# Optimization experiments

Hardware: AMD Instinct MI355X
Metric: run time of the kernel (lower is better)

## Reference

```python
import jax, jax.numpy as jnp
import numpy as np

DT = 0.05          # LiquidTimeBlock dt
EPS_TAU = 1e-6     # eps added to tau
EPS_CONV = 1e-3    # ContinuousRecurrentCore epsilon
MAX_T = 50         # max_sim_time
N_LAYERS = 4


def stable_sigmoid(v):
    # Sigmoid(x) == 0.5 * (tanh(x/2) + 1)
    return 0.5 * (jnp.tanh(v * 0.5) + 1.0)


def setup_inputs() -> dict:
    key = jax.random.key(0)
    B, S, H = 8, 1024, 1024
    ks = jax.random.split(key, 7)
    bnd = 1.0 / np.sqrt(H)      # nn.Linear default init bound, fan_in=H
    bnd2 = 1.0 / np.sqrt(2 * H)  # fan_in=2H for tau_gate
    x = jax.random.normal(ks[0], (B, S, H), jnp.float32)
    w_state = jax.random.uniform(ks[1], (N_LAYERS, H, H), jnp.float32, -bnd, bnd)
    b_state = jax.random.uniform(ks[2], (N_LAYERS, H), jnp.float32, -bnd, bnd)
    w_input = jax.random.uniform(ks[3], (N_LAYERS, H, H), jnp.float32, -bnd, bnd)
    b_input = jax.random.uniform(ks[4], (N_LAYERS, H), jnp.float32, -bnd, bnd)
    w_tau = jax.random.uniform(ks[5], (N_LAYERS, H, 2 * H), jnp.float32, -bnd2, bnd2)
    b_tau = jax.random.uniform(ks[6], (N_LAYERS, H), jnp.float32, -bnd2, bnd2)
    return {"x": x, "w_state": w_state, "b_state": b_state,
            "w_input": w_input, "b_input": b_input,
            "w_tau": w_tau, "b_tau": b_tau}


def reference(x, w_state, b_state, w_input, b_input, w_tau, b_tau):
    B, S, H = x.shape
    states0 = jnp.zeros((N_LAYERS, B, S, H), x.dtype)

    def step(carry, t):
        states, done, t_conv = carry
        cur = x
        new_states = []
        max_delta = jnp.zeros((), x.dtype)
        for i in range(N_LAYERS):  # fixed small structural loop
            h = states[i]
            combined = jnp.concatenate([cur, h], axis=-1)          # [B,S,2H]
            tau = stable_sigmoid(combined @ w_tau[i].T + b_tau[i])  # [B,S,H]
            forcing = jnp.tanh(h @ w_state[i].T + b_state[i]
                               + cur @ w_input[i].T + b_input[i])
            h_new = jnp.clip(h + DT * (-h / (tau + EPS_TAU) + forcing), -10.0, 10.0)
            max_delta = jnp.maximum(max_delta, jnp.max(jnp.abs(h_new - h)))
            new_states.append(h_new)
            cur = h_new
        nxt = jnp.stack(new_states)
        states = jnp.where(done, states, nxt)  # freeze after convergence
        conv = max_delta < EPS_CONV
        t_conv = jnp.where(jnp.logical_and(jnp.logical_not(done), conv), t, t_conv)
        done = jnp.logical_or(done, conv)
        return (states, done, t_conv), None

    init = (states0, jnp.array(False), jnp.array(MAX_T, jnp.int32))
    (states, done, t_conv), _ = jax.lax.scan(step, init, jnp.arange(MAX_T, dtype=jnp.int32))
    return states[-1], t_conv
```

## Files before the change

### kernel.cpp

```cpp
#include <hip/hip_runtime.h>
#include <hip/hip_bf16.h>


typedef __attribute__((ext_vector_type(8))) short bf16x8s;
typedef __attribute__((ext_vector_type(4))) float f32x4;

constexpr int HD = 1024;
constexpr int MR = 8192;
constexpr int NLAYER = 4;
constexpr int MAXT = 50;
constexpr float DTC = 0.05f;
constexpr float EPS_TAU_C = 1e-6f;
constexpr float EPS_CONV_C = 1e-3f;

constexpr int KSTORE = 2048;
constexpr int NPACK = 2048;
constexpr size_t WP_PER_LAYER = (size_t)(KSTORE / 64) * 16 * 128 * 64;
constexpr size_t HN = (size_t)MR * HD;

struct Ctrl {
  unsigned int done;
  int t_conv;
  unsigned int delta[MAXT];
};

__device__ __align__(16) __hip_bfloat16 g_Wp[NLAYER * WP_PER_LAYER];
__device__ __align__(16) __hip_bfloat16 g_xhi[HN];
__device__ __align__(16) __hip_bfloat16 g_xlo[HN];
__device__ __align__(16) __hip_bfloat16 g_h_hi[2 * NLAYER * HN];
__device__ __align__(16) __hip_bfloat16 g_h_lo[2 * NLAYER * HN];
__device__ float g_btau[NLAYER * HD];
__device__ float g_bforc[NLAYER * HD];
__device__ Ctrl g_ctrl;

__device__ __forceinline__ void gload_lds16(const __hip_bfloat16* g, __hip_bfloat16* lds) {
  __builtin_amdgcn_global_load_lds(
      (const __attribute__((address_space(1))) unsigned int*)g,
      (__attribute__((address_space(3))) unsigned int*)lds, 16, 0, 0);
}

__device__ __forceinline__ float fast_tanh(float x) {
  float t = __expf(-2.0f * fabsf(x));
  float r = __fdividef(1.0f - t, 1.0f + t);
  return copysignf(r, x);
}

__global__ void pack_weights(const float* __restrict__ w_state,
                             const float* __restrict__ w_input,
                             const float* __restrict__ w_tau,
                             const float* __restrict__ b_state,
                             const float* __restrict__ b_input,
                             const float* __restrict__ b_tau) {
  size_t idx = (size_t)blockIdx.x * blockDim.x + threadIdx.x;
  if (idx < (size_t)NLAYER * HD) {
    int l = (int)(idx >> 10), jj = (int)(idx & 1023);
    g_btau[idx]  = b_tau[l * HD + jj];
    g_bforc[idx] = b_state[l * HD + jj] + b_input[l * HD + jj];
  }
  const size_t total = (size_t)NLAYER * KSTORE * NPACK;
  if (idx >= total) return;
  int kk = (int)(idx & 63);  size_t r = idx >> 6;
  int nn = (int)(r & 127);   r >>= 7;
  int nt = (int)(r & 15);    r >>= 4;
  int kt = (int)(r & 31);
  int layer = (int)(r >> 5);
  int kg = kt * 64 + kk;
  int kb = kg >> 10;
  int k  = kg & 1023;
  int n  = nt * 128 + nn;
  int b  = n >> 4;
  int j  = (b >> 1) * 16 + (n & 15);
  bool is_tau = (b & 1) == 0;
  bool is_h   = (kb & 1) != 0;
  float wv;
  if (is_tau) wv = w_tau[(size_t)layer * HD * 2 * HD + (size_t)j * 2 * HD + (is_h ? HD + k : k)];
  else        wv = is_h ? w_state[(size_t)layer * HD * HD + (size_t)j * HD + k]
                        : w_input[(size_t)layer * HD * HD + (size_t)j * HD + k];
  g_Wp[idx] = __float2bfloat16(wv);
}

__global__ void split_x(const float* __restrict__ x) {
  size_t i = (size_t)blockIdx.x * blockDim.x + threadIdx.x;
  if (i >= HN) return;
  float v = x[i];
  __hip_bfloat16 h16 = __float2bfloat16(v);
  g_xhi[i] = h16;
  g_xlo[i] = __float2bfloat16(v - __bfloat162float(h16));
}

__global__ void zero_h() {
  const size_t nvec = (size_t)NLAYER * HN / 8;
  bf16x8s z = {};
  for (size_t i = (size_t)blockIdx.x * blockDim.x + threadIdx.x;
       i < nvec; i += (size_t)gridDim.x * blockDim.x) {
    ((bf16x8s*)g_h_hi)[i] = z;
    ((bf16x8s*)g_h_lo)[i] = z;
  }
}

__global__ void init_ctrl() {
  if (threadIdx.x == 0) { g_ctrl.done = 0u; g_ctrl.t_conv = MAXT; }
  if (threadIdx.x < MAXT) g_ctrl.delta[threadIdx.x] = 0u;
}

__launch_bounds__(256, 2)
__global__ void fused_step(int layer, int pin, int pout, int t) {
  if (g_ctrl.done) return;

  const __hip_bfloat16* cur_hi  = (layer == 0) ? g_xhi : &g_h_hi[((size_t)pout * NLAYER + (layer - 1)) * HN];
  const __hip_bfloat16* cur_lo  = (layer == 0) ? g_xlo : &g_h_lo[((size_t)pout * NLAYER + (layer - 1)) * HN];
  const __hip_bfloat16* h_hi_in = &g_h_hi[((size_t)pin * NLAYER + layer) * HN];
  const __hip_bfloat16* h_lo_in = &g_h_lo[((size_t)pin * NLAYER + layer) * HN];
  __hip_bfloat16* h_hi_out      = &g_h_hi[((size_t)pout * NLAYER + layer) * HN];
  __hip_bfloat16* h_lo_out      = &g_h_lo[((size_t)pout * NLAYER + layer) * HN];
  const __hip_bfloat16* Wpl     = &g_Wp[(size_t)layer * WP_PER_LAYER];
  const float* btau  = &g_btau[layer * HD];
  const float* bforc = &g_bforc[layer * HD];

  __shared__ __align__(16) __hip_bfloat16 Asm[128 * 64];
  __shared__ __align__(16) __hip_bfloat16 Bsm[128 * 64];

  const int tid  = threadIdx.x;
  const int lane = tid & 63;
  const int wave = tid >> 6;
  const int wm = wave >> 1, wn = wave & 1;
  const int m0 = blockIdx.x * 128;
  const int nt = blockIdx.y;

  f32x4 acc[4][4] = {};

  for (int kb = 0; kb < 4; ++kb) {
    const __hip_bfloat16* asrc;
    int sb;
    switch (kb) {
      case 0: asrc = cur_hi;  sb = 0; break;
      case 1: asrc = h_hi_in; sb = 1; break;
      case 2: asrc = cur_lo;  sb = 0; break;
      default: asrc = h_lo_in; sb = 1; break;
    }
    for (int t16 = 0; t16 < 16; ++t16) {
      const int kts = sb * 16 + t16;
      const int kcol = t16 * 64;
      #pragma unroll
      for (int i = 0; i < 4; ++i) {
        int g = wave * 4 + i;
        int row = g * 8 + (lane >> 3);
        gload_lds16(asrc + (size_t)(m0 + row) * HD + kcol + (lane & 7) * 8,
                    &Asm[g * 512]);
      }
      const __hip_bfloat16* bp = Wpl + ((size_t)kts * 16 + nt) * 8192;
      #pragma unroll
      for (int i = 0; i < 4; ++i) {
        int g = wave * 4 + i;
        gload_lds16(bp + g * 512 + lane * 8, &Bsm[g * 512]);
      }
      __syncthreads();
      #pragma unroll
      for (int ks = 0; ks < 2; ++ks) {
        const int k0 = ks * 32 + (lane >> 4) * 8;
        bf16x8s af[4], bfr[4];
        #pragma unroll
        for (int fm = 0; fm < 4; ++fm)
          af[fm] = *(const bf16x8s*)&Asm[(wm * 64 + fm * 16 + (lane & 15)) * 64 + k0];
        #pragma unroll
        for (int fn = 0; fn < 4; ++fn)
          bfr[fn] = *(const bf16x8s*)&Bsm[(wn * 64 + fn * 16 + (lane & 15)) * 64 + k0];
        #pragma unroll
        for (int fm = 0; fm < 4; ++fm)
          #pragma unroll
          for (int fn = 0; fn < 4; ++fn)
            acc[fm][fn] = __builtin_amdgcn_mfma_f32_16x16x32_bf16(
                af[fm], bfr[fn], acc[fm][fn], 0, 0, 0);
      }
      __syncthreads();
    }
  }

  float lmax = 0.0f;
  const int col = lane & 15;
  const int rbase = (lane >> 4) * 4;
  #pragma unroll
  for (int fm = 0; fm < 4; ++fm) {
    #pragma unroll
    for (int p = 0; p < 2; ++p) {
      const int j = nt * 64 + wn * 32 + p * 16 + col;
      const float bt = btau[j], bfo = bforc[j];
      f32x4 tp = acc[fm][2 * p];
      f32x4 fp = acc[fm][2 * p + 1];
      #pragma unroll
      for (int r2 = 0; r2 < 4; ++r2) {
        const int m = m0 + wm * 64 + fm * 16 + rbase + r2;
        const size_t off = (size_t)m * HD + j;
        float tau  = 0.5f * (fast_tanh(0.5f * (tp[r2] + bt)) + 1.0f);
        float forc = fast_tanh(fp[r2] + bfo);
        float hold = __bfloat162float(h_hi_in[off]) + __bfloat162float(h_lo_in[off]);
        float hn = hold + DTC * (-hold / (tau + EPS_TAU_C) + forc);
        hn = fminf(10.0f, fmaxf(-10.0f, hn));
        lmax = fmaxf(lmax, fabsf(hn - hold));
        __hip_bfloat16 hhi = __float2bfloat16(hn);
        h_hi_out[off] = hhi;
        h_lo_out[off] = __float2bfloat16(hn - __bfloat162float(hhi));
      }
    }
  }
  #pragma unroll
  for (int s = 32; s; s >>= 1) lmax = fmaxf(lmax, __shfl_xor(lmax, s, 64));
  if (lane == 0) atomicMax(&g_ctrl.delta[t], __float_as_uint(lmax));
}

__global__ void check_step(int t) {
  if (threadIdx.x != 0) return;
  if (g_ctrl.done) return;
  if (__uint_as_float(g_ctrl.delta[t]) < EPS_CONV_C) { g_ctrl.done = 1u; g_ctrl.t_conv = t; }
}

__global__ void write_out(float* __restrict__ out, int out_size) {
  size_t i = (size_t)blockIdx.x * blockDim.x + threadIdx.x;
  if (i >= (size_t)out_size) return;
  int tc = g_ctrl.t_conv;
  int last = (tc >= MAXT) ? (MAXT - 1) : tc;
  int par = (last + 1) & 1;
  const __hip_bfloat16* hh = &g_h_hi[((size_t)par * NLAYER + (NLAYER - 1)) * HN];
  const __hip_bfloat16* hl = &g_h_lo[((size_t)par * NLAYER + (NLAYER - 1)) * HN];
  if (i == (size_t)(out_size - 1)) {
    out[i] = (float)tc;
  } else if (i < HN) {
    out[i] = __bfloat162float(hh[i]) + __bfloat162float(hl[i]);
  }
}

extern "C" void kernel_launch(void* const* d_in, const int* in_sizes, int n_in,
                              void* d_out, int out_size, void* d_ws, size_t ws_size,
                              hipStream_t stream) {
  const float* x       = (const float*)d_in[0];
  const float* w_state = (const float*)d_in[1];
  const float* b_state = (const float*)d_in[2];
  const float* w_input = (const float*)d_in[3];
  const float* b_input = (const float*)d_in[4];
  const float* w_tau   = (const float*)d_in[5];
  const float* b_tau   = (const float*)d_in[6];
  (void)d_ws; (void)ws_size; (void)in_sizes; (void)n_in;

  {
    size_t total = (size_t)NLAYER * KSTORE * NPACK;
    pack_weights<<<dim3((unsigned)((total + 255) / 256)), dim3(256), 0, stream>>>(
        w_state, w_input, w_tau, b_state, b_input, b_tau);
  }
  split_x<<<dim3((unsigned)((HN + 255) / 256)), dim3(256), 0, stream>>>(x);
  zero_h<<<dim3(2048), dim3(256), 0, stream>>>();
  init_ctrl<<<dim3(1), dim3(64), 0, stream>>>();

  for (int t = 0; t < MAXT; ++t) {
    const int pin = t & 1, pout = 1 - pin;
    for (int l = 0; l < NLAYER; ++l) {
      fused_step<<<dim3(64, 16), dim3(256), 0, stream>>>(l, pin, pout, t);
    }
    check_step<<<dim3(1), dim3(64), 0, stream>>>(t);
  }

  write_out<<<dim3((unsigned)((HN + 256) / 256)), dim3(256), 0, stream>>>(
      (float*)d_out, out_size);
}
```

Before: 47.18 ms.

## Use 256x256 tiles with triple-buffered LDS pipeline in fused GEMM step

Replaces the 128x128, BK=64, single-buffered GEMM tile with a 256x256, BK=32 tile on 512 threads. Global-to-LDS loads are staged two iterations ahead across three buffers, with one barrier per k-step instead of two. MFMA blocks are issued at raised wave priority. Packed weights are relaid out to match the new tile shape. Larger tiles improve operand reuse, but the grid shrinks to 256 blocks, which may underfill the GPU's CUs, and register pressure rises.

```diff
diff --git a/kernel.cpp b/kernel.cpp
--- a/kernel.cpp
+++ b/kernel.cpp
@@ -13,9 +13,11 @@
 constexpr float EPS_TAU_C = 1e-6f;
 constexpr float EPS_CONV_C = 1e-3f;
 
+constexpr int BM = 256, BN = 256, BK = 32;
 constexpr int KSTORE = 2048;
 constexpr int NPACK = 2048;
-constexpr size_t WP_PER_LAYER = (size_t)(KSTORE / 64) * 16 * 128 * 64;
+constexpr int NKT = 128;
+constexpr size_t WP_PER_LAYER = (size_t)64 * 8 * BN * BK;
 constexpr size_t HN = (size_t)MR * HD;
 
 struct Ctrl {
@@ -59,23 +61,21 @@
   }
   const size_t total = (size_t)NLAYER * KSTORE * NPACK;
   if (idx >= total) return;
-  int kk = (int)(idx & 63);  size_t r = idx >> 6;
-  int nn = (int)(r & 127);   r >>= 7;
-  int nt = (int)(r & 15);    r >>= 4;
-  int kt = (int)(r & 31);
-  int layer = (int)(r >> 5);
-  int kg = kt * 64 + kk;
-  int kb = kg >> 10;
-  int k  = kg & 1023;
-  int n  = nt * 128 + nn;
+  int kk  = (int)(idx & 31);  size_t r = idx >> 5;
+  int nn  = (int)(r & 255);   r >>= 8;
+  int bnb = (int)(r & 7);     r >>= 3;
+  int kts = (int)(r & 63);    r >>= 6;
+  int layer = (int)r;
+  int kb = kts >> 5;
+  int k  = (kts & 31) * 32 + kk;
+  int n  = bnb * 256 + nn;
   int b  = n >> 4;
   int j  = (b >> 1) * 16 + (n & 15);
   bool is_tau = (b & 1) == 0;
-  bool is_h   = (kb & 1) != 0;
   float wv;
-  if (is_tau) wv = w_tau[(size_t)layer * HD * 2 * HD + (size_t)j * 2 * HD + (is_h ? HD + k : k)];
-  else        wv = is_h ? w_state[(size_t)layer * HD * HD + (size_t)j * HD + k]
-                        : w_input[(size_t)layer * HD * HD + (size_t)j * HD + k];
+  if (is_tau) wv = w_tau[(size_t)layer * HD * 2 * HD + (size_t)j * 2 * HD + (kb ? HD + k : k)];
+  else        wv = kb ? w_state[(size_t)layer * HD * HD + (size_t)j * HD + k]
+                      : w_input[(size_t)layer * HD * HD + (size_t)j * HD + k];
   g_Wp[idx] = __float2bfloat16(wv);
 }
 
@@ -103,7 +103,7 @@
   if (threadIdx.x < MAXT) g_ctrl.delta[threadIdx.x] = 0u;
 }
 
-__launch_bounds__(256, 2)
+__launch_bounds__(512, 2)
 __global__ void fused_step(int layer, int pin, int pout, int t) {
   if (g_ctrl.done) return;
 
@@ -117,79 +117,87 @@
   const float* btau  = &g_btau[layer * HD];
   const float* bforc = &g_bforc[layer * HD];
 
-  __shared__ __align__(16) __hip_bfloat16 Asm[128 * 64];
-  __shared__ __align__(16) __hip_bfloat16 Bsm[128 * 64];
+  __shared__ __align__(16) __hip_bfloat16 Asm3[3][BM * BK];
+  __shared__ __align__(16) __hip_bfloat16 Bsm3[3][BN * BK];
 
   const int tid  = threadIdx.x;
   const int lane = tid & 63;
   const int wave = tid >> 6;
-  const int wm = wave >> 1, wn = wave & 1;
-  const int m0 = blockIdx.x * 128;
-  const int nt = blockIdx.y;
-
-  f32x4 acc[4][4] = {};
-
-  for (int kb = 0; kb < 4; ++kb) {
+  const int wm = wave >> 2, wn = wave & 3;
+  const int m0 = blockIdx.x * BM;
+  const int bn = blockIdx.y;
+
+  auto stage = [&](int T, int b) {
     const __hip_bfloat16* asrc;
-    int sb;
-    switch (kb) {
-      case 0: asrc = cur_hi;  sb = 0; break;
-      case 1: asrc = h_hi_in; sb = 1; break;
-      case 2: asrc = cur_lo;  sb = 0; break;
-      default: asrc = h_lo_in; sb = 1; break;
-    }
-    for (int t16 = 0; t16 < 16; ++t16) {
-      const int kts = sb * 16 + t16;
-      const int kcol = t16 * 64;
+    int pass = T >> 5;
+    switch (pass) {
+      case 0: asrc = cur_hi;  break;
+      case 1: asrc = h_hi_in; break;
+      case 2: asrc = cur_lo;  break;
+      default: asrc = h_lo_in; break;
+    }
+    const int kcol = (T & 31) * BK;
+    const int kts = ((pass & 1) << 5) + (T & 31);
+    const __hip_bfloat16* bp = Wpl + ((size_t)kts * 8 + bn) * (BN * BK);
+    #pragma unroll
+    for (int L = 0; L < 2; ++L) {
+      const int c = L * 8 + wave;
+      gload_lds16(asrc + (size_t)(m0 + c * 16 + (lane >> 2)) * HD + kcol + (lane & 3) * 8,
+                  &Asm3[b][c * 512]);
+      gload_lds16(bp + c * 512 + lane * 8, &Bsm3[b][c * 512]);
+    }
+  };
+
+  f32x4 acc[8][4] = {};
+
+  auto compute = [&](int b) {
+    bf16x8s af[8], bfr[4];
+    const int rsel = lane & 15, k0 = (lane >> 4) * 8;
+    #pragma unroll
+    for (int fm = 0; fm < 8; ++fm)
+      af[fm] = *(const bf16x8s*)&Asm3[b][(wm * 128 + fm * 16 + rsel) * BK + k0];
+    #pragma unroll
+    for (int fn = 0; fn < 4; ++fn)
+      bfr[fn] = *(const bf16x8s*)&Bsm3[b][(wn * 64 + fn * 16 + rsel) * BK + k0];
+    __builtin_amdgcn_s_setprio(1);
+    #pragma unroll
+    for (int fm = 0; fm < 8; ++fm)
       #pragma unroll
-      for (int i = 0; i < 4; ++i) {
-        int g = wave * 4 + i;
-        int row = g * 8 + (lane >> 3);
-        gload_lds16(asrc + (size_t)(m0 + row) * HD + kcol + (lane & 7) * 8,
-                    &Asm[g * 512]);
-      }
-      const __hip_bfloat16* bp = Wpl + ((size_t)kts * 16 + nt) * 8192;
-      #pragma unroll
-      for (int i = 0; i < 4; ++i) {
-        int g = wave * 4 + i;
-        gload_lds16(bp + g * 512 + lane * 8, &Bsm[g * 512]);
-      }
-      __syncthreads();
-      #pragma unroll
-      for (int ks = 0; ks < 2; ++ks) {
-        const int k0 = ks * 32 + (lane >> 4) * 8;
-        bf16x8s af[4], bfr[4];
-        #pragma unroll
-        for (int fm = 0; fm < 4; ++fm)
-          af[fm] = *(const bf16x8s*)&Asm[(wm * 64 + fm * 16 + (lane & 15)) * 64 + k0];
-        #pragma unroll
-        for (int fn = 0; fn < 4; ++fn)
-          bfr[fn] = *(const bf16x8s*)&Bsm[(wn * 64 + fn * 16 + (lane & 15)) * 64 + k0];
-        #pragma unroll
-        for (int fm = 0; fm < 4; ++fm)
-          #pragma unroll
-          for (int fn = 0; fn < 4; ++fn)
-            acc[fm][fn] = __builtin_amdgcn_mfma_f32_16x16x32_bf16(
-                af[fm], bfr[fn], acc[fm][fn], 0, 0, 0);
-      }
-      __syncthreads();
-    }
-  }
+      for (int fn = 0; fn < 4; ++fn)
+        acc[fm][fn] = __builtin_amdgcn_mfma_f32_16x16x32_bf16(
+            af[fm], bfr[fn], acc[fm][fn], 0, 0, 0);
+    __builtin_amdgcn_s_setprio(0);
+  };
+
+  stage(0, 0);
+  stage(1, 1);
+
+  for (int T = 0; T < NKT - 1; ++T) {
+    asm volatile("s_waitcnt vmcnt(4)" ::: "memory");
+    __builtin_amdgcn_s_barrier();
+    __builtin_amdgcn_sched_barrier(0);
+    if (T < NKT - 2) stage(T + 2, (T + 2) % 3);
+    compute(T % 3);
+  }
+  asm volatile("s_waitcnt vmcnt(0)" ::: "memory");
+  __builtin_amdgcn_s_barrier();
+  __builtin_amdgcn_sched_barrier(0);
+  compute((NKT - 1) % 3);
 
   float lmax = 0.0f;
   const int col = lane & 15;
   const int rbase = (lane >> 4) * 4;
   #pragma unroll
-  for (int fm = 0; fm < 4; ++fm) {
+  for (int fm = 0; fm < 8; ++fm) {
     #pragma unroll
     for (int p = 0; p < 2; ++p) {
-      const int j = nt * 64 + wn * 32 + p * 16 + col;
+      const int j = (bn * 8 + wn * 2 + p) * 16 + col;
       const float bt = btau[j], bfo = bforc[j];
       f32x4 tp = acc[fm][2 * p];
       f32x4 fp = acc[fm][2 * p + 1];
       #pragma unroll
       for (int r2 = 0; r2 < 4; ++r2) {
-        const int m = m0 + wm * 64 + fm * 16 + rbase + r2;
+        const int m = m0 + wm * 128 + fm * 16 + rbase + r2;
         const size_t off = (size_t)m * HD + j;
         float tau  = 0.5f * (fast_tanh(0.5f * (tp[r2] + bt)) + 1.0f);
         float forc = fast_tanh(fp[r2] + bfo);
@@ -253,7 +261,7 @@
   for (int t = 0; t < MAXT; ++t) {
     const int pin = t & 1, pout = 1 - pin;
     for (int l = 0; l < NLAYER; ++l) {
-      fused_step<<<dim3(64, 16), dim3(256), 0, stream>>>(l, pin, pout, t);
+      fused_step<<<dim3(32, 8), dim3(512), 0, stream>>>(l, pin, pout, t);
     }
     check_step<<<dim3(1), dim3(64), 0, stream>>>(t);
   }
```

Result: slower. 49.45 ms (+4.8%).
